# Performance work log

Hardware: AMD Instinct MI355X
Metric: run time of the kernel (lower is better)

The kernel has to match this reference:

```python
import jax, jax.numpy as jnp
import numpy as np

D_MIN, D_MAX, D_COUNT = 2.0, 22.0, 36  # RFdiffusion rbf() constants


def _rbf(D):
    # D: [..., L, L] -> [..., L, L, D_COUNT]
    mu = jnp.linspace(D_MIN, D_MAX, D_COUNT, dtype=D.dtype)
    sigma = (D_MAX - D_MIN) / D_COUNT
    return jnp.exp(-(((D[..., None] - mu) / sigma) ** 2))


def _layernorm(x, w, b, eps=1e-5):
    mu = jnp.mean(x, axis=-1, keepdims=True)
    var = jnp.var(x, axis=-1, keepdims=True)
    return (x - mu) * jax.lax.rsqrt(var + eps) * w + b


def setup_inputs() -> dict:
    key = jax.random.key(0)
    ks = jax.random.split(key, 8)
    B, L, d_state, d_pair, h, d_rbf = 1, 512, 256, 128, 32, D_COUNT
    s = lambda d: 1.0 / np.sqrt(d)
    return {
        "xyz": jax.random.normal(ks[0], (B, L, 3, 3), jnp.float32) * 5.0,
        "state": jax.random.normal(ks[1], (B, L, d_state), jnp.float32),
        "ln_w": jnp.ones((d_state,), jnp.float32),
        "ln_b": jnp.zeros((d_state,), jnp.float32),
        "w_rbf": jax.random.normal(ks[2], (d_rbf, d_pair), jnp.float32) * s(d_rbf),
        "b_rbf": jnp.zeros((d_pair,), jnp.float32),
        "w_left": jax.random.normal(ks[3], (d_state, h), jnp.float32) * s(d_state),
        "b_left": jnp.zeros((h,), jnp.float32),
        "w_right": jax.random.normal(ks[4], (d_state, h), jnp.float32) * s(d_state),
        "b_right": jnp.zeros((h,), jnp.float32),
        "w_gate": jax.random.normal(ks[5], (h * h, d_pair), jnp.float32) * s(h * h),
        "b_gate": jnp.zeros((d_pair,), jnp.float32),
    }


def reference(xyz, state, ln_w, ln_b, w_rbf, b_rbf, w_left, b_left,
              w_right, b_right, w_gate, b_gate):
    B, L = xyz.shape[:2]
    h = w_left.shape[1]
    d_pair = w_rbf.shape[1]

    # pairwise CA distances -> RBF features -> project to pair dim
    cas = xyz[:, :, 1]                                        # [B, L, 3]
    d2 = jnp.sum((cas[:, :, None, :] - cas[:, None, :, :]) ** 2, axis=-1)
    dist = jnp.sqrt(jnp.maximum(d2, 1e-12))                   # [B, L, L]
    rbf_feat = _rbf(dist) @ w_rbf + b_rbf                     # [B, L, L, d_pair]

    # gated pair bias: sigmoid(to_gate(outer(left, right)))
    st = _layernorm(state, ln_w, ln_b)
    left = st @ w_left + b_left                               # [B, L, h]
    right = st @ w_right + b_right                            # [B, L, h]

    # Algebraically identical to einsum('bli,bmj->blmij') -> reshape -> Linear,
    # but factored through the projection weight to avoid the O(L^2 h^2) tensor.
    Wg = w_gate.reshape(h, h, d_pair)                         # flatten order i*h+j
    t = jnp.einsum('bli,ijp->bljp', left, Wg)                 # [B, L, h, d_pair]
    logits = jnp.einsum('bljp,bmj->blmp', t, right) + b_gate  # [B, L, L, d_pair]
    gate = jax.nn.sigmoid(logits)

    return gate * rbf_feat
```

## Files before the change

### kernel.cpp

```cpp
#include <hip/hip_runtime.h>
#include <hip/hip_fp16.h>

typedef _Float16 half8 __attribute__((ext_vector_type(8)));
typedef float floatx4 __attribute__((ext_vector_type(4)));

#define LSEQ 512
#define DSTATE 256
#define DPAIR 128
#define HH 32
#define DRBF 36

#define MUSTEP (20.0f / 35.0f)
#define INVSIG 1.8f

__global__ __launch_bounds__(256) void prologA(
    const float* __restrict__ state, const float* __restrict__ ln_w,
    const float* __restrict__ ln_b, const float* __restrict__ w_left,
    const float* __restrict__ b_left, const float* __restrict__ w_right,
    const float* __restrict__ b_right, float* __restrict__ left,
    _Float16* __restrict__ right_h) {
  __shared__ float stS[DSTATE];
  __shared__ float redS[4], redQ[4];
  const int l = blockIdx.x, tid = threadIdx.x;

  float x = state[l * DSTATE + tid];
  float s = x, q = x * x;
  #pragma unroll
  for (int o = 32; o > 0; o >>= 1) {
    s += __shfl_down(s, o);
    q += __shfl_down(q, o);
  }
  if ((tid & 63) == 0) { redS[tid >> 6] = s; redQ[tid >> 6] = q; }
  __syncthreads();
  float tot = redS[0] + redS[1] + redS[2] + redS[3];
  float totq = redQ[0] + redQ[1] + redQ[2] + redQ[3];
  float mean = tot * (1.0f / DSTATE);
  float var = totq * (1.0f / DSTATE) - mean * mean;
  float inv = rsqrtf(var + 1e-5f);
  stS[tid] = (x - mean) * inv * ln_w[tid] + ln_b[tid];
  __syncthreads();

  if (tid < HH) {
    float acc = b_left[tid];
    for (int c = 0; c < DSTATE; ++c) acc += stS[c] * w_left[c * HH + tid];
    left[l * HH + tid] = acc;
  } else if (tid >= 64 && tid < 64 + HH) {
    const int j = tid - 64;
    float acc = b_right[j];
    for (int c = 0; c < DSTATE; ++c) acc += stS[c] * w_right[c * HH + j];
    right_h[l * HH + j] = (_Float16)acc;
  }
}

__global__ __launch_bounds__(256) void prologB(
    const float* __restrict__ w_gate, const float* __restrict__ w_rbf,
    const float* __restrict__ left, _Float16* __restrict__ tT,
    _Float16* __restrict__ w_rbfT) {
  const int tid = threadIdx.x;
  if (blockIdx.x == 128) {
    for (int e = tid; e < DPAIR * 64; e += 256) {
      int p = e >> 6, k = e & 63;
      w_rbfT[e] = (k < DRBF) ? (_Float16)w_rbf[k * DPAIR + p] : (_Float16)0.0f;
    }
    return;
  }
  const int c = blockIdx.x & 15;
  const int lc = blockIdx.x >> 4;
  const int j = tid & 31;
  const int p = c * 8 + (tid >> 5);

  float wcol[32];
  #pragma unroll
  for (int i = 0; i < 32; ++i) wcol[i] = w_gate[(i * HH + j) * DPAIR + p];

  const int l0 = lc * 64;
  for (int l = l0; l < l0 + 64; ++l) {
    const float* __restrict__ lf = left + l * HH;
    float acc = 0.0f;
    #pragma unroll
    for (int i = 0; i < 32; ++i) acc += lf[i] * wcol[i];
    tT[l * (DPAIR * HH) + c * 256 + tid] = (_Float16)acc;
  }
}

__global__ __launch_bounds__(256, 3) void mainC(
    const float* __restrict__ xyz, const float* __restrict__ b_rbf,
    const float* __restrict__ b_gate, const _Float16* __restrict__ right_h,
    const _Float16* __restrict__ tT, const _Float16* __restrict__ w_rbfT,
    float* __restrict__ out) {
  const int l = blockIdx.x >> 1;
  const int half = blockIdx.x & 1;
  const int tid = threadIdx.x;
  const int wave = tid >> 6;
  const int lane = tid & 63;
  const int ln16 = lane & 15;
  const int quad = lane >> 4;

  const float clx = xyz[l * 9 + 3];
  const float cly = xyz[l * 9 + 4];
  const float clz = xyz[l * 9 + 5];

  half8 Bt[8], Bw0[8], Bw1[8];
  float bg[8], br[8];
  const _Float16* tTl = tT + (size_t)l * (DPAIR * HH);
  #pragma unroll
  for (int pt = 0; pt < 8; ++pt) {
    const int p = pt * 16 + ln16;
    Bt[pt] = *(const half8*)(tTl + p * HH + quad * 8);
    Bw0[pt] = *(const half8*)(w_rbfT + p * 64 + quad * 8);
    Bw1[pt] = *(const half8*)(w_rbfT + p * 64 + 32 + quad * 8);
    bg[pt] = b_gate[p];
    br[pt] = b_rbf[p];
  }

  const int mt0 = half * 16;
  for (int mt = mt0 + wave; mt < mt0 + 16; mt += 4) {
    const int mA = mt * 16 + ln16;
    half8 Ar = *(const half8*)(right_h + mA * HH + quad * 8);

    const float dx = clx - xyz[mA * 9 + 3];
    const float dy = cly - xyz[mA * 9 + 4];
    const float dz = clz - xyz[mA * 9 + 5];
    const float d = sqrtf(fmaxf(dx * dx + dy * dy + dz * dz, 1e-12f));

    half8 A0, A1;
    #pragma unroll
    for (int jj = 0; jj < 8; ++jj) {
      const int k = quad * 8 + jj;
      const float u = (d - (2.0f + (float)k * MUSTEP)) * INVSIG;
      A0[jj] = (_Float16)__expf(-u * u);
    }
    #pragma unroll
    for (int jj = 0; jj < 8; ++jj) {
      const int k = 32 + quad * 8 + jj;
      float v = 0.0f;
      if (k < DRBF) {
        const float u = (d - (2.0f + (float)k * MUSTEP)) * INVSIG;
        v = __expf(-u * u);
      }
      A1[jj] = (_Float16)v;
    }

    #pragma unroll
    for (int pt = 0; pt < 8; ++pt) {
      floatx4 accL = {0.f, 0.f, 0.f, 0.f};
      floatx4 accR = {0.f, 0.f, 0.f, 0.f};
      accL = __builtin_amdgcn_mfma_f32_16x16x32_f16(Ar, Bt[pt], accL, 0, 0, 0);
      accR = __builtin_amdgcn_mfma_f32_16x16x32_f16(A0, Bw0[pt], accR, 0, 0, 0);
      accR = __builtin_amdgcn_mfma_f32_16x16x32_f16(A1, Bw1[pt], accR, 0, 0, 0);

      const int p = pt * 16 + ln16;
      float* orow = out + ((size_t)l * LSEQ + mt * 16 + quad * 4) * DPAIR + p;
      #pragma unroll
      for (int i = 0; i < 4; ++i) {
        const float logit = accL[i] + bg[pt];
        const float gate = __builtin_amdgcn_rcpf(1.0f + __expf(-logit));
        const float feat = accR[i] + br[pt];
        orow[i * DPAIR] = gate * feat;
      }
    }
  }
}

extern "C" void kernel_launch(void* const* d_in, const int* in_sizes, int n_in,
                              void* d_out, int out_size, void* d_ws,
                              size_t ws_size, hipStream_t stream) {
  const float* xyz = (const float*)d_in[0];
  const float* state = (const float*)d_in[1];
  const float* ln_w = (const float*)d_in[2];
  const float* ln_b = (const float*)d_in[3];
  const float* w_rbf = (const float*)d_in[4];
  const float* b_rbf = (const float*)d_in[5];
  const float* w_left = (const float*)d_in[6];
  const float* b_left = (const float*)d_in[7];
  const float* w_right = (const float*)d_in[8];
  const float* b_right = (const float*)d_in[9];
  const float* w_gate = (const float*)d_in[10];
  const float* b_gate = (const float*)d_in[11];
  float* out = (float*)d_out;

  char* ws = (char*)d_ws;
  float* left = (float*)ws;
  _Float16* right_h = (_Float16*)(ws + 65536);
  _Float16* tT = (_Float16*)(ws + 98304);
  _Float16* w_rbfT = (_Float16*)(ws + 4292608);

  prologA<<<512, 256, 0, stream>>>(state, ln_w, ln_b, w_left, b_left, w_right,
                                   b_right, left, right_h);
  prologB<<<129, 256, 0, stream>>>(w_gate, w_rbf, left, tT, w_rbfT);
  mainC<<<1024, 256, 0, stream>>>(xyz, b_rbf, b_gate, right_h, tT, w_rbfT, out);
}
```

Before: 192.9 us.

## Parallelize prolog projections and stage main-kernel B operands in LDS

prologA now uses all 256 threads to compute left/right projections via a 4-way split over input channels with a shared-memory reduction. prologB launches 8x more blocks, each handling 8 rows instead of 64, to fill the GPU. mainC copies the per-row tT slice and the transposed RBF weights into LDS and reads MFMA B fragments from there per tile instead of holding 24 half8 registers. This reduces register pressure and serial prolog work, at the cost of LDS traffic, a block barrier, and dropping the occupancy hint.

```diff
diff --git a/kernel.cpp b/kernel.cpp
--- a/kernel.cpp
+++ b/kernel.cpp
@@ -21,6 +21,7 @@
     _Float16* __restrict__ right_h) {
   __shared__ float stS[DSTATE];
   __shared__ float redS[4], redQ[4];
+  __shared__ float part[4][64];
   const int l = blockIdx.x, tid = threadIdx.x;
 
   float x = state[l * DSTATE + tid];
@@ -40,15 +41,21 @@
   stS[tid] = (x - mean) * inv * ln_w[tid] + ln_b[tid];
   __syncthreads();
 
-  if (tid < HH) {
-    float acc = b_left[tid];
-    for (int c = 0; c < DSTATE; ++c) acc += stS[c] * w_left[c * HH + tid];
-    left[l * HH + tid] = acc;
-  } else if (tid >= 64 && tid < 64 + HH) {
-    const int j = tid - 64;
-    float acc = b_right[j];
-    for (int c = 0; c < DSTATE; ++c) acc += stS[c] * w_right[c * HH + j];
-    right_h[l * HH + j] = (_Float16)acc;
+  const int j = tid & 63;
+  const int quarter = tid >> 6;
+  const float* __restrict__ w = (j < HH) ? (w_left + j) : (w_right + (j - HH));
+  const int c0 = quarter * 64;
+  float acc = 0.0f;
+  #pragma unroll 8
+  for (int cc = 0; cc < 64; ++cc) acc += stS[c0 + cc] * w[(c0 + cc) * HH];
+  part[quarter][j] = acc;
+  __syncthreads();
+  if (tid < 64) {
+    float sum = part[0][tid] + part[1][tid] + part[2][tid] + part[3][tid];
+    if (tid < HH)
+      left[l * HH + tid] = sum + b_left[tid];
+    else
+      right_h[l * HH + (tid - HH)] = (_Float16)(sum + b_right[tid - HH]);
   }
 }
 
@@ -57,7 +64,7 @@
     const float* __restrict__ left, _Float16* __restrict__ tT,
     _Float16* __restrict__ w_rbfT) {
   const int tid = threadIdx.x;
-  if (blockIdx.x == 128) {
+  if (blockIdx.x == 1024) {
     for (int e = tid; e < DPAIR * 64; e += 256) {
       int p = e >> 6, k = e & 63;
       w_rbfT[e] = (k < DRBF) ? (_Float16)w_rbf[k * DPAIR + p] : (_Float16)0.0f;
@@ -73,8 +80,9 @@
   #pragma unroll
   for (int i = 0; i < 32; ++i) wcol[i] = w_gate[(i * HH + j) * DPAIR + p];
 
-  const int l0 = lc * 64;
-  for (int l = l0; l < l0 + 64; ++l) {
+  const int l0 = lc * 8;
+  #pragma unroll
+  for (int l = l0; l < l0 + 8; ++l) {
     const float* __restrict__ lf = left + l * HH;
     float acc = 0.0f;
     #pragma unroll
@@ -83,11 +91,13 @@
   }
 }
 
-__global__ __launch_bounds__(256, 3) void mainC(
+__global__ __launch_bounds__(256) void mainC(
     const float* __restrict__ xyz, const float* __restrict__ b_rbf,
     const float* __restrict__ b_gate, const _Float16* __restrict__ right_h,
     const _Float16* __restrict__ tT, const _Float16* __restrict__ w_rbfT,
     float* __restrict__ out) {
+  __shared__ _Float16 sT[DPAIR * HH];
+  __shared__ _Float16 sW[DPAIR * 64];
   const int l = blockIdx.x >> 1;
   const int half = blockIdx.x & 1;
   const int tid = threadIdx.x;
@@ -96,22 +106,29 @@
   const int ln16 = lane & 15;
   const int quad = lane >> 4;
 
+  {
+    const uint4* __restrict__ src = (const uint4*)(tT + (size_t)l * (DPAIR * HH));
+    uint4* dst = (uint4*)sT;
+    #pragma unroll
+    for (int i = 0; i < 2; ++i) dst[tid + 256 * i] = src[tid + 256 * i];
+    const uint4* __restrict__ src2 = (const uint4*)w_rbfT;
+    uint4* dst2 = (uint4*)sW;
+    #pragma unroll
+    for (int i = 0; i < 4; ++i) dst2[tid + 256 * i] = src2[tid + 256 * i];
+  }
+
   const float clx = xyz[l * 9 + 3];
   const float cly = xyz[l * 9 + 4];
   const float clz = xyz[l * 9 + 5];
 
-  half8 Bt[8], Bw0[8], Bw1[8];
   float bg[8], br[8];
-  const _Float16* tTl = tT + (size_t)l * (DPAIR * HH);
   #pragma unroll
   for (int pt = 0; pt < 8; ++pt) {
-    const int p = pt * 16 + ln16;
-    Bt[pt] = *(const half8*)(tTl + p * HH + quad * 8);
-    Bw0[pt] = *(const half8*)(w_rbfT + p * 64 + quad * 8);
-    Bw1[pt] = *(const half8*)(w_rbfT + p * 64 + 32 + quad * 8);
-    bg[pt] = b_gate[p];
-    br[pt] = b_rbf[p];
-  }
+    bg[pt] = b_gate[pt * 16 + ln16];
+    br[pt] = b_rbf[pt * 16 + ln16];
+  }
+
+  __syncthreads();
 
   const int mt0 = half * 16;
   for (int mt = mt0 + wave; mt < mt0 + 16; mt += 4) {
@@ -143,13 +160,17 @@
 
     #pragma unroll
     for (int pt = 0; pt < 8; ++pt) {
+      const int p = pt * 16 + ln16;
+      half8 Bt = *(const half8*)(sT + p * HH + quad * 8);
+      half8 Bw0 = *(const half8*)(sW + p * 64 + quad * 8);
+      half8 Bw1 = *(const half8*)(sW + p * 64 + 32 + quad * 8);
+
       floatx4 accL = {0.f, 0.f, 0.f, 0.f};
       floatx4 accR = {0.f, 0.f, 0.f, 0.f};
-      accL = __builtin_amdgcn_mfma_f32_16x16x32_f16(Ar, Bt[pt], accL, 0, 0, 0);
-      accR = __builtin_amdgcn_mfma_f32_16x16x32_f16(A0, Bw0[pt], accR, 0, 0, 0);
-      accR = __builtin_amdgcn_mfma_f32_16x16x32_f16(A1, Bw1[pt], accR, 0, 0, 0);
-
-      const int p = pt * 16 + ln16;
+      accL = __builtin_amdgcn_mfma_f32_16x16x32_f16(Ar, Bt, accL, 0, 0, 0);
+      accR = __builtin_amdgcn_mfma_f32_16x16x32_f16(A0, Bw0, accR, 0, 0, 0);
+      accR = __builtin_amdgcn_mfma_f32_16x16x32_f16(A1, Bw1, accR, 0, 0, 0);
+
       float* orow = out + ((size_t)l * LSEQ + mt * 16 + quad * 4) * DPAIR + p;
       #pragma unroll
       for (int i = 0; i < 4; ++i) {
@@ -187,6 +208,6 @@
 
   prologA<<<512, 256, 0, stream>>>(state, ln_w, ln_b, w_left, b_left, w_right,
                                    b_right, left, right_h);
-  prologB<<<129, 256, 0, stream>>>(w_gate, w_rbf, left, tT, w_rbfT);
+  prologB<<<1025, 256, 0, stream>>>(w_gate, w_rbf, left, tT, w_rbfT);
   mainC<<<1024, 256, 0, stream>>>(xyz, b_rbf, b_gate, right_h, tT, w_rbfT, out);
 }
```

New measurement: 190.2 us. No clear change (-1.4%).
